# Optimization experiments

Measured on AMD Instinct MI355X. Metric: run time of the kernel, lower is better.

Reference implementation:

```python
import jax, jax.numpy as jnp
import numpy as np

NUM_HEADS = 32
NUM_KV_HEADS = 8
HEAD_DIM = 128
N_REP = NUM_HEADS // NUM_KV_HEADS
BLOCK = 256  # kvcache_block_size
NUM_BLOCKS = 32
BATCH = 4
SEQ = 1024
N_TOK = BATCH * SEQ

# scale is computed in the torch module as (1/sqrt(head_dim)) rounded to bfloat16
SCALE = jnp.float32(jnp.asarray(1.0 / np.sqrt(HEAD_DIM), dtype=jnp.bfloat16))


def setup_inputs() -> dict:
    key = jax.random.key(0)
    kq, kk, kv = jax.random.split(key, 3)
    q = jax.random.normal(kq, (N_TOK, NUM_HEADS, HEAD_DIM), dtype=jnp.float32)
    k = jax.random.normal(kk, (N_TOK, NUM_KV_HEADS, HEAD_DIM), dtype=jnp.float32)
    v = jax.random.normal(kv, (N_TOK, NUM_KV_HEADS, HEAD_DIM), dtype=jnp.float32)
    k_cache = jnp.zeros((NUM_BLOCKS, BLOCK, NUM_KV_HEADS, HEAD_DIM), dtype=jnp.float32)
    v_cache = jnp.zeros_like(k_cache)
    slot_mapping = jnp.arange(N_TOK, dtype=jnp.int64 if jax.config.jax_enable_x64 else jnp.int32)
    cu = jnp.arange(BATCH + 1, dtype=jnp.int32) * SEQ
    return {"q": q, "k": k, "v": v, "k_cache": k_cache, "v_cache": v_cache,
            "slot_mapping": slot_mapping, "cu_seqlens_q": cu, "cu_seqlens_k": cu}


def _store_kvcache(k, v, k_cache, v_cache, slot_mapping):
    # scatter store of new K/V into paged cache; invalid slots are dropped
    blk = slot_mapping // BLOCK
    inner = slot_mapping % BLOCK
    valid = (slot_mapping != -1) & (blk < k_cache.shape[0]) & (inner < BLOCK)
    blk = jnp.where(valid, blk, k_cache.shape[0])  # out-of-range -> dropped
    k_cache = k_cache.at[blk, inner].set(k, mode="drop")
    v_cache = v_cache.at[blk, inner].set(v, mode="drop")
    return k_cache, v_cache


def _prefill_attn(q, k, v):
    # packed varlen batch with uniform seq lengths -> dense [B,S,...] causal GQA attention
    qb = q.reshape(BATCH, SEQ, NUM_HEADS, HEAD_DIM)
    kb = jnp.repeat(k.reshape(BATCH, SEQ, NUM_KV_HEADS, HEAD_DIM), N_REP, axis=2)  # repeat_kv
    vb = jnp.repeat(v.reshape(BATCH, SEQ, NUM_KV_HEADS, HEAD_DIM), N_REP, axis=2)
    scores = jnp.einsum("bqhd,bkhd->bhqk", qb, kb) * SCALE  # [B,H,S,S]
    causal = jnp.tril(jnp.ones((SEQ, SEQ), dtype=bool))
    scores = jnp.where(causal, scores, -jnp.inf)
    # torch code clamps to [-100, 100] before softmax (masked -inf becomes -100)
    probs = jax.nn.softmax(jnp.clip(scores, -100.0, 100.0), axis=-1)
    out = jnp.einsum("bhqk,bkhd->bqhd", probs, vb)
    return out.reshape(N_TOK, NUM_HEADS * HEAD_DIM)


def reference(q, k, v, k_cache, v_cache, slot_mapping, cu_seqlens_q, cu_seqlens_k):
    k_cache, v_cache = _store_kvcache(k, v, k_cache, v_cache, slot_mapping)
    o = _prefill_attn(q, k, v)
    return o, k_cache, v_cache
```

## Files before the change

### kernel.cpp

```cpp
#include <hip/hip_runtime.h>
#include <math.h>
#include <string.h>

#define BB 4
#define SS 1024
#define HH 32
#define GG 8
#define DD 128
#define NTOK (BB*SS)
#define NBLK 32
#define BLKSZ 256
#define CACHE_ELEMS ((size_t)NBLK*BLKSZ*GG*DD)

typedef __attribute__((ext_vector_type(8)))  short  short8;
typedef __attribute__((ext_vector_type(16))) float  floatx16;

union FragU { unsigned u[4]; uint4 u4; short8 s8; };

typedef __attribute__((address_space(3))) void  lds_void;
typedef __attribute__((address_space(1))) const void glb_void;

__device__ __forceinline__ unsigned pack_bf16x2(float a, float b) {
    unsigned ua = __builtin_bit_cast(unsigned, a);
    unsigned ub = __builtin_bit_cast(unsigned, b);
    ua = (ua + 0x7FFFu + ((ua >> 16) & 1u)) >> 16;
    ub = (ub + 0x7FFFu + ((ub >> 16) & 1u)) & 0xFFFF0000u;
    return ua | ub;
}

__global__ void swizzle_kv(const float* __restrict__ k, const float* __restrict__ v,
                           uint4* __restrict__ ksw, uint4* __restrict__ vsw) {
    __shared__ float lds[32 * 132];
    const int t = threadIdx.x;
    const int kt = blockIdx.x, gy = blockIdx.y, b = blockIdx.z;
    const int isv = gy >> 3, g = gy & 7;
    const float* sp = (isv ? v : k) + ((size_t)(b * SS + kt * 32) * GG + g) * DD;
    #pragma unroll
    for (int i = 0; i < 4; ++i) {
        int u = t + 256 * i;
        int row = u >> 5, c4 = u & 31;
        float4 f = *(const float4*)(sp + (size_t)row * (GG * DD) + c4 * 4);
        float* lp = &lds[row * 132 + c4 * 4];
        lp[0] = f.x; lp[1] = f.y; lp[2] = f.z; lp[3] = f.w;
    }
    __syncthreads();
    const int lane = t & 63, hb = lane >> 5, l31 = lane & 31;
    const size_t tbase = ((size_t)(b * GG + g) * 32 + kt) * 8;
    if (!isv) {
        #pragma unroll
        for (int i = 0; i < 2; ++i) {
            int s = (t >> 6) + 4 * i;
            const float* lp = &lds[l31 * 132 + s * 16 + hb * 8];
            uint4 o;
            o.x = pack_bf16x2(lp[0], lp[1]); o.y = pack_bf16x2(lp[2], lp[3]);
            o.z = pack_bf16x2(lp[4], lp[5]); o.w = pack_bf16x2(lp[6], lp[7]);
            ksw[(tbase + s) * 64 + lane] = o;
        }
    } else {
        #pragma unroll
        for (int i = 0; i < 2; ++i) {
            int f8 = (t >> 6) + 4 * i;
            int t4 = f8 >> 1, s2 = f8 & 1;
            int keyb = s2 * 16 + hb * 8;
            int d = t4 * 32 + l31;
            uint4 o;
            o.x = pack_bf16x2(lds[(keyb + 0) * 132 + d], lds[(keyb + 1) * 132 + d]);
            o.y = pack_bf16x2(lds[(keyb + 2) * 132 + d], lds[(keyb + 3) * 132 + d]);
            o.z = pack_bf16x2(lds[(keyb + 4) * 132 + d], lds[(keyb + 5) * 132 + d]);
            o.w = pack_bf16x2(lds[(keyb + 6) * 132 + d], lds[(keyb + 7) * 132 + d]);
            vsw[(tbase + f8) * 64 + lane] = o;
        }
    }
}

__global__ void copy_cache2(const float4* __restrict__ s0, const float4* __restrict__ s1,
                            float4* __restrict__ d0, float4* __restrict__ d1) {
    const size_t half = CACHE_ELEMS / 4;
    size_t i = (size_t)blockIdx.x * 256 + threadIdx.x;
    if (i < half) d0[i] = s0[i];
    else          d1[i - half] = s1[i - half];
}

__global__ void scatter_kernel(const float* __restrict__ k, const float* __restrict__ v,
                               const int* __restrict__ slot_mapping,
                               float* __restrict__ kco, float* __restrict__ vco) {
    const int tok = blockIdx.x, c = threadIdx.x;
    const int slot = slot_mapping[tok];
    if (slot < 0 || slot >= NBLK * BLKSZ) return;
    float4 kf = ((const float4*)(k + (size_t)tok * 1024))[c];
    float4 vf = ((const float4*)(v + (size_t)tok * 1024))[c];
    ((float4*)(kco + (size_t)slot * 1024))[c] = kf;
    ((float4*)(vco + (size_t)slot * 1024))[c] = vf;
}

__global__ __launch_bounds__(256, 3)
void attn_kernel(const float* __restrict__ q,
                 const uint4* __restrict__ ksw,
                 const uint4* __restrict__ vsw,
                 float* __restrict__ out, float sc2 ) {
    __shared__ uint4 sm[2][16][64];
    const int lane = threadIdx.x & 63;
    const int wave = threadIdx.x >> 6;
    const int l31  = lane & 31;
    const int hb   = lane >> 5;
    const int qt = (int)(gridDim.x - 1) - (int)blockIdx.x;
    const int g = blockIdx.y, b = blockIdx.z;
    const int h  = g * 4 + wave;
    const int q0 = qt * 32;
    const int tb = b * SS;

    const uint4* kpl = ksw + (size_t)(b * GG + g) * (32 * 8 * 64);
    const uint4* vpl = vsw + (size_t)(b * GG + g) * (32 * 8 * 64);

    #pragma unroll
    for (int i = 0; i < 2; ++i) {
        int row = wave * 2 + i;
        __builtin_amdgcn_global_load_lds((glb_void*)(kpl + row * 64 + lane),
                                         (lds_void*)(&sm[0][row][0]),     16, 0, 0);
        __builtin_amdgcn_global_load_lds((glb_void*)(vpl + row * 64 + lane),
                                         (lds_void*)(&sm[0][8 + row][0]), 16, 0, 0);
    }

    short8 qf[8];
    const float* qp = q + ((size_t)(tb + q0 + l31) * HH + h) * DD;
    #pragma unroll
    for (int s = 0; s < 8; ++s) {
        int d0 = s * 16 + hb * 8;
        float4 f0 = *(const float4*)(qp + d0);
        float4 f1 = *(const float4*)(qp + d0 + 4);
        FragU fr;
        fr.u[0] = pack_bf16x2(f0.x, f0.y); fr.u[1] = pack_bf16x2(f0.z, f0.w);
        fr.u[2] = pack_bf16x2(f1.x, f1.y); fr.u[3] = pack_bf16x2(f1.z, f1.w);
        qf[s] = fr.s8;
    }

    floatx16 oacc[4] = {};
    float m = -__builtin_inff(), l = 0.f;

    __syncthreads();

    for (int kt = 0; kt <= qt; ++kt) {
        const int cur = kt & 1;
        if (kt < qt) {
            const uint4* gk = kpl + (kt + 1) * 512;
            const uint4* gv = vpl + (kt + 1) * 512;
            #pragma unroll
            for (int i = 0; i < 2; ++i) {
                int row = wave * 2 + i;
                __builtin_amdgcn_global_load_lds((glb_void*)(gk + row * 64 + lane),
                                                 (lds_void*)(&sm[cur ^ 1][row][0]),     16, 0, 0);
                __builtin_amdgcn_global_load_lds((glb_void*)(gv + row * 64 + lane),
                                                 (lds_void*)(&sm[cur ^ 1][8 + row][0]), 16, 0, 0);
            }
        }
        floatx16 st0 = {}, st1 = {};
        #pragma unroll
        for (int s = 0; s < 4; ++s) {
            FragU ka; ka.u4 = sm[cur][s][lane];
            st0 = __builtin_amdgcn_mfma_f32_32x32x16_bf16(ka.s8, qf[s], st0, 0, 0, 0);
            FragU kb; kb.u4 = sm[cur][s + 4][lane];
            st1 = __builtin_amdgcn_mfma_f32_32x32x16_bf16(kb.s8, qf[s + 4], st1, 0, 0, 0);
        }
        float e[16];
        #pragma unroll
        for (int r = 0; r < 16; ++r) {
            float val = (st0[r] + st1[r]) * sc2;
            if (kt == qt) {
                int row = (r & 3) + 8 * (r >> 2) + 4 * hb;
                if (row > l31) val = -__builtin_inff();
            }
            e[r] = val;
        }
        float tr[8];
        #pragma unroll
        for (int i = 0; i < 8; ++i) tr[i] = fmaxf(e[i], e[i + 8]);
        #pragma unroll
        for (int i = 0; i < 4; ++i) tr[i] = fmaxf(tr[i], tr[i + 4]);
        tr[0] = fmaxf(tr[0], tr[2]); tr[1] = fmaxf(tr[1], tr[3]);
        float tmax = fmaxf(tr[0], tr[1]);
        tmax = fmaxf(tmax, __shfl_xor(tmax, 32));
        const float mnew  = fmaxf(m, tmax);
        const float alpha = exp2f(m - mnew);
        float p[16];
        #pragma unroll
        for (int r = 0; r < 16; ++r) p[r] = exp2f(e[r] - mnew);
        float sr[8];
        #pragma unroll
        for (int i = 0; i < 8; ++i) sr[i] = p[i] + p[i + 8];
        #pragma unroll
        for (int i = 0; i < 4; ++i) sr[i] += sr[i + 4];
        float psum = (sr[0] + sr[1]) + (sr[2] + sr[3]);
        psum += __shfl_xor(psum, 32);
        if (__any(tmax > m)) {
            #pragma unroll
            for (int t = 0; t < 4; ++t)
                #pragma unroll
                for (int r = 0; r < 16; ++r) oacc[t][r] *= alpha;
        }
        l = l * alpha + psum;
        m = mnew;
        unsigned pk[8], px[8];
        #pragma unroll
        for (int u2 = 0; u2 < 8; ++u2) pk[u2] = pack_bf16x2(p[2*u2], p[2*u2+1]);
        #pragma unroll
        for (int u2 = 0; u2 < 8; ++u2) px[u2] = (unsigned)__shfl_xor((int)pk[u2], 32);
        #pragma unroll
        for (int s2 = 0; s2 < 2; ++s2) {
            FragU pf;
            if (hb == 0) { pf.u[0]=pk[4*s2  ]; pf.u[1]=pk[4*s2+1]; pf.u[2]=px[4*s2  ]; pf.u[3]=px[4*s2+1]; }
            else         { pf.u[0]=px[4*s2+2]; pf.u[1]=px[4*s2+3]; pf.u[2]=pk[4*s2+2]; pf.u[3]=pk[4*s2+3]; }
            #pragma unroll
            for (int t = 0; t < 4; ++t) {
                FragU vf; vf.u4 = sm[cur][8 + t * 2 + s2][lane];
                oacc[t] = __builtin_amdgcn_mfma_f32_32x32x16_bf16(vf.s8, pf.s8, oacc[t], 0, 0, 0);
            }
        }
        __syncthreads();
    }
    const float inv_l = 1.f / l;
    float* op = out + ((size_t)(tb + q0 + l31) * HH + h) * DD;
    #pragma unroll
    for (int t = 0; t < 4; ++t) {
        #pragma unroll
        for (int grp = 0; grp < 4; ++grp) {
            float4 o4;
            o4.x = oacc[t][grp*4+0] * inv_l; o4.y = oacc[t][grp*4+1] * inv_l;
            o4.z = oacc[t][grp*4+2] * inv_l; o4.w = oacc[t][grp*4+3] * inv_l;
            *(float4*)(op + t * 32 + grp * 8 + hb * 4) = o4;
        }
    }
}

extern "C" void kernel_launch(void* const* d_in, const int* in_sizes, int n_in,
                              void* d_out, int out_size, void* d_ws, size_t ws_size,
                              hipStream_t stream) {
    const float* q     = (const float*)d_in[0];
    const float* k     = (const float*)d_in[1];
    const float* v     = (const float*)d_in[2];
    const float* kc_in = (const float*)d_in[3];
    const float* vc_in = (const float*)d_in[4];
    const int*   slot  = (const int*)d_in[5];

    float* o_out  = (float*)d_out;
    float* kc_out = o_out + (size_t)NTOK * HH * DD;
    float* vc_out = kc_out + CACHE_ELEMS;

    uint4* ksw = (uint4*)d_ws;
    uint4* vsw = ksw + (size_t)BB * GG * 32 * 8 * 64;

    float sc = 1.0f / sqrtf((float)DD);
    unsigned u; memcpy(&u, &sc, 4);
    u = (u + 0x7FFFu + ((u >> 16) & 1u)) & 0xFFFF0000u;
    memcpy(&sc, &u, 4);
    const float sc2 = sc * 1.44269504088896340736f;

    swizzle_kv<<<dim3(32, GG * 2, BB), 256, 0, stream>>>(k, v, ksw, vsw);
    copy_cache2<<<(int)(CACHE_ELEMS / 4 / 256) * 2, 256, 0, stream>>>(
        (const float4*)kc_in, (const float4*)vc_in, (float4*)kc_out, (float4*)vc_out);
    scatter_kernel<<<NTOK, 256, 0, stream>>>(k, v, slot, kc_out, vc_out);
    attn_kernel<<<dim3(SS / 32, GG, BB), 256, 0, stream>>>(q, ksw, vsw, o_out, sc2);
}
```

Baseline: 367.6 us.

## Fuse KV scatter into swizzle, pair causal tiles per block, lazy rescale

The KV cache scatter is folded into the bf16 swizzle kernel, which removes one launch and a second read of K/V. The attention grid becomes 512 blocks. Each block handles two query tiles (qt and 31-qt) to even out causal work, and blocks are mapped per XCD so a batch-head's K/V stays in that XCD's cache. Inside the loop, the two partial score accumulators become one MFMA chain and scaling is folded into an FMA before exp2. The running max is only rescaled when it grows by more than 8, and cross-half reductions and the P fragment exchange use permlane32_swap with hardware bf16 pack and setprio around the MFMA blocks. Launch bounds drop to 2 waves per SIMD, and the lazy rescale trades a bounded exp2 range for fewer accumulator rescales.

```diff
diff --git a/kernel.cpp b/kernel.cpp
--- a/kernel.cpp
+++ b/kernel.cpp
@@ -28,13 +28,47 @@
     return ua | ub;
 }
 
-__global__ void swizzle_kv(const float* __restrict__ k, const float* __restrict__ v,
-                           uint4* __restrict__ ksw, uint4* __restrict__ vsw) {
+#if __has_builtin(__builtin_amdgcn_permlane32_swap)
+#define HAVE_PL32 1
+#endif
+
+__device__ __forceinline__ unsigned cvt_pk_bf16(float lo, float hi) {
+    unsigned r;
+    asm("v_cvt_pk_bf16_f32 %0, %1, %2" : "=v"(r) : "v"(lo), "v"(hi));
+    return r;
+}
+
+__device__ __forceinline__ float xhalf_max(float x) {
+#ifdef HAVE_PL32
+    unsigned u = __builtin_bit_cast(unsigned, x);
+    auto r = __builtin_amdgcn_permlane32_swap(u, u, false, false);
+    return fmaxf(__builtin_bit_cast(float, (unsigned)r[0]),
+                 __builtin_bit_cast(float, (unsigned)r[1]));
+#else
+    return fmaxf(x, __shfl_xor(x, 32));
+#endif
+}
+__device__ __forceinline__ float xhalf_add(float x) {
+#ifdef HAVE_PL32
+    unsigned u = __builtin_bit_cast(unsigned, x);
+    auto r = __builtin_amdgcn_permlane32_swap(u, u, false, false);
+    return __builtin_bit_cast(float, (unsigned)r[0]) +
+           __builtin_bit_cast(float, (unsigned)r[1]);
+#else
+    return x + __shfl_xor(x, 32);
+#endif
+}
+
+__global__ void prep_kv(const float* __restrict__ k, const float* __restrict__ v,
+                        const int* __restrict__ slot_mapping,
+                        uint4* __restrict__ ksw, uint4* __restrict__ vsw,
+                        float* __restrict__ kco, float* __restrict__ vco) {
     __shared__ float lds[32 * 132];
     const int t = threadIdx.x;
     const int kt = blockIdx.x, gy = blockIdx.y, b = blockIdx.z;
     const int isv = gy >> 3, g = gy & 7;
     const float* sp = (isv ? v : k) + ((size_t)(b * SS + kt * 32) * GG + g) * DD;
+    float* dco = isv ? vco : kco;
     #pragma unroll
     for (int i = 0; i < 4; ++i) {
         int u = t + 256 * i;
@@ -42,6 +76,9 @@
         float4 f = *(const float4*)(sp + (size_t)row * (GG * DD) + c4 * 4);
         float* lp = &lds[row * 132 + c4 * 4];
         lp[0] = f.x; lp[1] = f.y; lp[2] = f.z; lp[3] = f.w;
+        int slot = slot_mapping[b * SS + kt * 32 + row];
+        if ((unsigned)slot < (unsigned)(NBLK * BLKSZ))
+            *(float4*)(dco + (size_t)slot * (GG * DD) + g * DD + c4 * 4) = f;
     }
     __syncthreads();
     const int lane = t & 63, hb = lane >> 5, l31 = lane & 31;
@@ -81,19 +118,7 @@
     else          d1[i - half] = s1[i - half];
 }
 
-__global__ void scatter_kernel(const float* __restrict__ k, const float* __restrict__ v,
-                               const int* __restrict__ slot_mapping,
-                               float* __restrict__ kco, float* __restrict__ vco) {
-    const int tok = blockIdx.x, c = threadIdx.x;
-    const int slot = slot_mapping[tok];
-    if (slot < 0 || slot >= NBLK * BLKSZ) return;
-    float4 kf = ((const float4*)(k + (size_t)tok * 1024))[c];
-    float4 vf = ((const float4*)(v + (size_t)tok * 1024))[c];
-    ((float4*)(kco + (size_t)slot * 1024))[c] = kf;
-    ((float4*)(vco + (size_t)slot * 1024))[c] = vf;
-}
-
-__global__ __launch_bounds__(256, 3)
+__global__ __launch_bounds__(256, 2)
 void attn_kernel(const float* __restrict__ q,
                  const uint4* __restrict__ ksw,
                  const uint4* __restrict__ vsw,
@@ -103,130 +128,156 @@
     const int wave = threadIdx.x >> 6;
     const int l31  = lane & 31;
     const int hb   = lane >> 5;
-    const int qt = (int)(gridDim.x - 1) - (int)blockIdx.x;
-    const int g = blockIdx.y, b = blockIdx.z;
-    const int h  = g * 4 + wave;
-    const int q0 = qt * 32;
-    const int tb = b * SS;
-
-    const uint4* kpl = ksw + (size_t)(b * GG + g) * (32 * 8 * 64);
-    const uint4* vpl = vsw + (size_t)(b * GG + g) * (32 * 8 * 64);
-
-    #pragma unroll
-    for (int i = 0; i < 2; ++i) {
-        int row = wave * 2 + i;
-        __builtin_amdgcn_global_load_lds((glb_void*)(kpl + row * 64 + lane),
-                                         (lds_void*)(&sm[0][row][0]),     16, 0, 0);
-        __builtin_amdgcn_global_load_lds((glb_void*)(vpl + row * 64 + lane),
-                                         (lds_void*)(&sm[0][8 + row][0]), 16, 0, 0);
-    }
-
-    short8 qf[8];
-    const float* qp = q + ((size_t)(tb + q0 + l31) * HH + h) * DD;
-    #pragma unroll
-    for (int s = 0; s < 8; ++s) {
-        int d0 = s * 16 + hb * 8;
-        float4 f0 = *(const float4*)(qp + d0);
-        float4 f1 = *(const float4*)(qp + d0 + 4);
-        FragU fr;
-        fr.u[0] = pack_bf16x2(f0.x, f0.y); fr.u[1] = pack_bf16x2(f0.z, f0.w);
-        fr.u[2] = pack_bf16x2(f1.x, f1.y); fr.u[3] = pack_bf16x2(f1.z, f1.w);
-        qf[s] = fr.s8;
-    }
-
-    floatx16 oacc[4] = {};
-    float m = -__builtin_inff(), l = 0.f;
-
-    __syncthreads();
-
-    for (int kt = 0; kt <= qt; ++kt) {
-        const int cur = kt & 1;
-        if (kt < qt) {
-            const uint4* gk = kpl + (kt + 1) * 512;
-            const uint4* gv = vpl + (kt + 1) * 512;
-            #pragma unroll
-            for (int i = 0; i < 2; ++i) {
-                int row = wave * 2 + i;
-                __builtin_amdgcn_global_load_lds((glb_void*)(gk + row * 64 + lane),
-                                                 (lds_void*)(&sm[cur ^ 1][row][0]),     16, 0, 0);
-                __builtin_amdgcn_global_load_lds((glb_void*)(gv + row * 64 + lane),
-                                                 (lds_void*)(&sm[cur ^ 1][8 + row][0]), 16, 0, 0);
-            }
-        }
-        floatx16 st0 = {}, st1 = {};
-        #pragma unroll
-        for (int s = 0; s < 4; ++s) {
-            FragU ka; ka.u4 = sm[cur][s][lane];
-            st0 = __builtin_amdgcn_mfma_f32_32x32x16_bf16(ka.s8, qf[s], st0, 0, 0, 0);
-            FragU kb; kb.u4 = sm[cur][s + 4][lane];
-            st1 = __builtin_amdgcn_mfma_f32_32x32x16_bf16(kb.s8, qf[s + 4], st1, 0, 0, 0);
-        }
-        float e[16];
-        #pragma unroll
-        for (int r = 0; r < 16; ++r) {
-            float val = (st0[r] + st1[r]) * sc2;
-            if (kt == qt) {
-                int row = (r & 3) + 8 * (r >> 2) + 4 * hb;
-                if (row > l31) val = -__builtin_inff();
-            }
-            e[r] = val;
-        }
-        float tr[8];
-        #pragma unroll
-        for (int i = 0; i < 8; ++i) tr[i] = fmaxf(e[i], e[i + 8]);
-        #pragma unroll
-        for (int i = 0; i < 4; ++i) tr[i] = fmaxf(tr[i], tr[i + 4]);
-        tr[0] = fmaxf(tr[0], tr[2]); tr[1] = fmaxf(tr[1], tr[3]);
-        float tmax = fmaxf(tr[0], tr[1]);
-        tmax = fmaxf(tmax, __shfl_xor(tmax, 32));
-        const float mnew  = fmaxf(m, tmax);
-        const float alpha = exp2f(m - mnew);
-        float p[16];
-        #pragma unroll
-        for (int r = 0; r < 16; ++r) p[r] = exp2f(e[r] - mnew);
-        float sr[8];
-        #pragma unroll
-        for (int i = 0; i < 8; ++i) sr[i] = p[i] + p[i + 8];
-        #pragma unroll
-        for (int i = 0; i < 4; ++i) sr[i] += sr[i + 4];
-        float psum = (sr[0] + sr[1]) + (sr[2] + sr[3]);
-        psum += __shfl_xor(psum, 32);
-        if (__any(tmax > m)) {
-            #pragma unroll
-            for (int t = 0; t < 4; ++t)
+
+    const int wg  = blockIdx.x;
+    const int xcd = wg & 7;
+    const int sl  = wg >> 3;
+    const int bg  = xcd * 4 + (sl >> 4);
+    const int pr  = sl & 15;
+    const int b   = bg >> 3, g = bg & 7;
+    const int h   = g * 4 + wave;
+    const int tb  = b * SS;
+
+    const uint4* kpl = ksw + (size_t)bg * (32 * 8 * 64);
+    const uint4* vpl = vsw + (size_t)bg * (32 * 8 * 64);
+
+    #pragma unroll 1
+    for (int half = 0; half < 2; ++half) {
+        const int qt = half ? pr : (31 - pr);
+        const int q0 = qt * 32;
+
+        #pragma unroll
+        for (int i = 0; i < 2; ++i) {
+            int row = wave * 2 + i;
+            __builtin_amdgcn_global_load_lds((glb_void*)(kpl + row * 64 + lane),
+                                             (lds_void*)(&sm[0][row][0]),     16, 0, 0);
+            __builtin_amdgcn_global_load_lds((glb_void*)(vpl + row * 64 + lane),
+                                             (lds_void*)(&sm[0][8 + row][0]), 16, 0, 0);
+        }
+
+        short8 qf[8];
+        const float* qp = q + ((size_t)(tb + q0 + l31) * HH + h) * DD;
+        #pragma unroll
+        for (int s = 0; s < 8; ++s) {
+            int d0 = s * 16 + hb * 8;
+            float4 f0 = *(const float4*)(qp + d0);
+            float4 f1 = *(const float4*)(qp + d0 + 4);
+            FragU fr;
+            fr.u[0] = pack_bf16x2(f0.x, f0.y); fr.u[1] = pack_bf16x2(f0.z, f0.w);
+            fr.u[2] = pack_bf16x2(f1.x, f1.y); fr.u[3] = pack_bf16x2(f1.z, f1.w);
+            qf[s] = fr.s8;
+        }
+
+        floatx16 oacc[4] = {};
+        float m = -__builtin_inff(), l = 0.f;
+
+        __syncthreads();
+
+        for (int kt = 0; kt <= qt; ++kt) {
+            const int cur = kt & 1;
+            if (kt < qt) {
+                const uint4* gk = kpl + (kt + 1) * 512;
+                const uint4* gv = vpl + (kt + 1) * 512;
                 #pragma unroll
-                for (int r = 0; r < 16; ++r) oacc[t][r] *= alpha;
-        }
-        l = l * alpha + psum;
-        m = mnew;
-        unsigned pk[8], px[8];
-        #pragma unroll
-        for (int u2 = 0; u2 < 8; ++u2) pk[u2] = pack_bf16x2(p[2*u2], p[2*u2+1]);
-        #pragma unroll
-        for (int u2 = 0; u2 < 8; ++u2) px[u2] = (unsigned)__shfl_xor((int)pk[u2], 32);
-        #pragma unroll
-        for (int s2 = 0; s2 < 2; ++s2) {
-            FragU pf;
-            if (hb == 0) { pf.u[0]=pk[4*s2  ]; pf.u[1]=pk[4*s2+1]; pf.u[2]=px[4*s2  ]; pf.u[3]=px[4*s2+1]; }
-            else         { pf.u[0]=px[4*s2+2]; pf.u[1]=px[4*s2+3]; pf.u[2]=pk[4*s2+2]; pf.u[3]=pk[4*s2+3]; }
-            #pragma unroll
-            for (int t = 0; t < 4; ++t) {
-                FragU vf; vf.u4 = sm[cur][8 + t * 2 + s2][lane];
-                oacc[t] = __builtin_amdgcn_mfma_f32_32x32x16_bf16(vf.s8, pf.s8, oacc[t], 0, 0, 0);
-            }
-        }
-        __syncthreads();
-    }
-    const float inv_l = 1.f / l;
-    float* op = out + ((size_t)(tb + q0 + l31) * HH + h) * DD;
-    #pragma unroll
-    for (int t = 0; t < 4; ++t) {
-        #pragma unroll
-        for (int grp = 0; grp < 4; ++grp) {
-            float4 o4;
-            o4.x = oacc[t][grp*4+0] * inv_l; o4.y = oacc[t][grp*4+1] * inv_l;
-            o4.z = oacc[t][grp*4+2] * inv_l; o4.w = oacc[t][grp*4+3] * inv_l;
-            *(float4*)(op + t * 32 + grp * 8 + hb * 4) = o4;
+                for (int i = 0; i < 2; ++i) {
+                    int row = wave * 2 + i;
+                    __builtin_amdgcn_global_load_lds((glb_void*)(gk + row * 64 + lane),
+                                                     (lds_void*)(&sm[cur ^ 1][row][0]),     16, 0, 0);
+                    __builtin_amdgcn_global_load_lds((glb_void*)(gv + row * 64 + lane),
+                                                     (lds_void*)(&sm[cur ^ 1][8 + row][0]), 16, 0, 0);
+                }
+            }
+            floatx16 st = {};
+            __builtin_amdgcn_s_setprio(1);
+            #pragma unroll
+            for (int s = 0; s < 8; ++s) {
+                FragU ka; ka.u4 = sm[cur][s][lane];
+                st = __builtin_amdgcn_mfma_f32_32x32x16_bf16(ka.s8, qf[s], st, 0, 0, 0);
+            }
+            __builtin_amdgcn_s_setprio(0);
+
+            float e[16];
+            #pragma unroll
+            for (int r = 0; r < 16; ++r) {
+                float val = st[r];
+                if (kt == qt) {
+                    int row = (r & 3) + 8 * (r >> 2) + 4 * hb;
+                    if (row > l31) val = -__builtin_inff();
+                }
+                e[r] = val;
+            }
+            float trm[8];
+            #pragma unroll
+            for (int i = 0; i < 8; ++i) trm[i] = fmaxf(e[i], e[i + 8]);
+            #pragma unroll
+            for (int i = 0; i < 4; ++i) trm[i] = fmaxf(trm[i], trm[i + 4]);
+            float tmax = fmaxf(fmaxf(trm[0], trm[2]), fmaxf(trm[1], trm[3]));
+            tmax = xhalf_max(tmax) * sc2;
+
+            if (__any(tmax > m + 8.f)) {
+                const float mnew  = fmaxf(m, tmax);
+                const float alpha = exp2f(m - mnew);
+                #pragma unroll
+                for (int t = 0; t < 4; ++t)
+                    #pragma unroll
+                    for (int r = 0; r < 16; ++r) oacc[t][r] *= alpha;
+                l *= alpha;
+                m = mnew;
+            }
+
+            float p_[16];
+            #pragma unroll
+            for (int r = 0; r < 16; ++r) p_[r] = exp2f(fmaf(e[r], sc2, -m));
+            float sr[8];
+            #pragma unroll
+            for (int i = 0; i < 8; ++i) sr[i] = p_[i] + p_[i + 8];
+            #pragma unroll
+            for (int i = 0; i < 4; ++i) sr[i] += sr[i + 4];
+            float psum = (sr[0] + sr[1]) + (sr[2] + sr[3]);
+            l += xhalf_add(psum);
+
+            unsigned pk[8];
+            #pragma unroll
+            for (int u2 = 0; u2 < 8; ++u2) pk[u2] = cvt_pk_bf16(p_[2 * u2], p_[2 * u2 + 1]);
+
+            __builtin_amdgcn_s_setprio(1);
+            #pragma unroll
+            for (int s2 = 0; s2 < 2; ++s2) {
+                FragU pf;
+#ifdef HAVE_PL32
+                auto ra = __builtin_amdgcn_permlane32_swap(pk[4 * s2],     pk[4 * s2 + 2], false, false);
+                auto rb = __builtin_amdgcn_permlane32_swap(pk[4 * s2 + 1], pk[4 * s2 + 3], false, false);
+                pf.u[0] = (unsigned)ra[0]; pf.u[1] = (unsigned)rb[0];
+                pf.u[2] = (unsigned)ra[1]; pf.u[3] = (unsigned)rb[1];
+#else
+                unsigned px0 = (unsigned)__shfl_xor((int)pk[4 * s2],     32);
+                unsigned px1 = (unsigned)__shfl_xor((int)pk[4 * s2 + 1], 32);
+                unsigned px2 = (unsigned)__shfl_xor((int)pk[4 * s2 + 2], 32);
+                unsigned px3 = (unsigned)__shfl_xor((int)pk[4 * s2 + 3], 32);
+                if (hb == 0) { pf.u[0] = pk[4*s2];   pf.u[1] = pk[4*s2+1]; pf.u[2] = px0; pf.u[3] = px1; }
+                else         { pf.u[0] = px2; pf.u[1] = px3; pf.u[2] = pk[4*s2+2]; pf.u[3] = pk[4*s2+3]; }
+#endif
+                #pragma unroll
+                for (int t = 0; t < 4; ++t) {
+                    FragU vf; vf.u4 = sm[cur][8 + t * 2 + s2][lane];
+                    oacc[t] = __builtin_amdgcn_mfma_f32_32x32x16_bf16(vf.s8, pf.s8, oacc[t], 0, 0, 0);
+                }
+            }
+            __builtin_amdgcn_s_setprio(0);
+            __syncthreads();
+        }
+
+        const float inv_l = 1.f / l;
+        float* op = out + ((size_t)(tb + q0 + l31) * HH + h) * DD;
+        #pragma unroll
+        for (int t = 0; t < 4; ++t) {
+            #pragma unroll
+            for (int grp = 0; grp < 4; ++grp) {
+                float4 o4;
+                o4.x = oacc[t][grp * 4 + 0] * inv_l; o4.y = oacc[t][grp * 4 + 1] * inv_l;
+                o4.z = oacc[t][grp * 4 + 2] * inv_l; o4.w = oacc[t][grp * 4 + 3] * inv_l;
+                *(float4*)(op + t * 32 + grp * 8 + hb * 4) = o4;
+            }
         }
     }
 }
@@ -254,9 +305,8 @@
     memcpy(&sc, &u, 4);
     const float sc2 = sc * 1.44269504088896340736f;
 
-    swizzle_kv<<<dim3(32, GG * 2, BB), 256, 0, stream>>>(k, v, ksw, vsw);
     copy_cache2<<<(int)(CACHE_ELEMS / 4 / 256) * 2, 256, 0, stream>>>(
         (const float4*)kc_in, (const float4*)vc_in, (float4*)kc_out, (float4*)vc_out);
-    scatter_kernel<<<NTOK, 256, 0, stream>>>(k, v, slot, kc_out, vc_out);
-    attn_kernel<<<dim3(SS / 32, GG, BB), 256, 0, stream>>>(q, ksw, vsw, o_out, sc2);
-}
+    prep_kv<<<dim3(32, GG * 2, BB), 256, 0, stream>>>(k, v, slot, ksw, vsw, kc_out, vc_out);
+    attn_kernel<<<512, 256, 0, stream>>>(q, ksw, vsw, o_out, sc2);
+}
```

Measured after the change: 311.4 us. 1.18x faster.
